# Optimization experiments

Measured on AMD Instinct MI355X. Metric: run time of the kernel, lower is better.

The kernel has to match this reference:

```python
import jax, jax.numpy as jnp
import numpy as np

N_NODES = 50000
N_EDGES = 800000
IN_CH, HID_CH, OUT_CH = 128, 128, 40


def setup_inputs() -> dict:
    key = jax.random.key(0)
    k1, k2, k3, k4 = jax.random.split(key, 4)
    x = jax.random.normal(k1, (N_NODES, IN_CH), dtype=jnp.float32)
    edge_index = jax.random.randint(k2, (2, N_EDGES), 0, N_NODES, dtype=jnp.int64)
    # Glorot-ish init for linear weights
    W1 = jax.random.normal(k3, (IN_CH, HID_CH), dtype=jnp.float32) / np.sqrt(IN_CH)
    b1 = jnp.zeros((HID_CH,), dtype=jnp.float32)
    W2 = jax.random.normal(k4, (HID_CH, OUT_CH), dtype=jnp.float32) / np.sqrt(HID_CH)
    b2 = jnp.zeros((OUT_CH,), dtype=jnp.float32)
    return {"x": x, "edge_index": edge_index, "W1": W1, "b1": b1, "W2": W2, "b2": b2}


def _gcn_conv(x, src, dst, W, b):
    # GCNConv(normalize=False): dense transform then sparse aggregation (scatter-add)
    h = x @ W                                   # [N, C_out]
    out = jax.ops.segment_sum(h[src], dst, num_segments=N_NODES)  # sum_{j->i} h[j]
    return out + b


def reference(x, edge_index, W1, b1, W2, b2):
    src, dst = edge_index[0], edge_index[1]
    h = _gcn_conv(x, src, dst, W1, b1)
    h = jax.nn.relu(h)
    # dropout is identity in eval mode
    h = _gcn_conv(h, src, dst, W2, b2)
    return jax.nn.log_softmax(h, axis=-1)
```

## Files before the change

kernel.cpp:

```cpp
#include <hip/hip_runtime.h>

#define NN 50000
#define NE 800000
#define NBKT 196
#define NBLK 256
#define EPB (NE / NBLK)
#define MATN (NBKT * NBLK)

using short8 = __attribute__((ext_vector_type(8))) short;
using f32x4  = __attribute__((ext_vector_type(4))) float;
union U4S8 { uint4 u; short8 v; };

__device__ __forceinline__ float lof(unsigned v) { return __uint_as_float(v << 16); }
__device__ __forceinline__ float hif(unsigned v) { return __uint_as_float(v & 0xffff0000u); }
__device__ __forceinline__ unsigned bf16rne(float f) {
    unsigned u = __float_as_uint(f);
    return (u + 0x7fffu + ((u >> 16) & 1u)) >> 16;
}
__device__ __forceinline__ unsigned pack2(float a, float b) {
    return bf16rne(a) | (bf16rne(b) << 16);
}
__device__ __forceinline__ unsigned fp8pack4(float a0, float a1, float a2, float a3) {
    int w = __builtin_amdgcn_cvt_pk_fp8_f32(a0, a1, 0, false);
    w = __builtin_amdgcn_cvt_pk_fp8_f32(a2, a3, w, true);
    return (unsigned)w;
}

__global__ __launch_bounds__(256) void binhist_k(const int* __restrict__ dst,
                                                 int* __restrict__ mat,
                                                 const float* __restrict__ W1,
                                                 const float* __restrict__ W2,
                                                 unsigned* __restrict__ W1T,
                                                 unsigned* __restrict__ W2T) {
    __shared__ int hist[NBKT];
    const int tid = threadIdx.x;
    for (int i = tid; i < NBKT; i += 256) hist[i] = 0;

    const int g = blockIdx.x * 256 + tid;
    if (g < 8192) {
        const int n = g >> 6, k2 = (g & 63) * 2;
        W1T[g] = pack2(W1[k2 * 128 + n], W1[(k2 + 1) * 128 + n]);
    } else if (g < 8192 + 3072) {
        const int u = g - 8192;
        const int n = u >> 6;
        const int q0 = (u & 63) * 2, q1 = q0 + 1;
        const int c0 = (q0 & 7) * 16 + (q0 >> 3);
        const int c1 = (q1 & 7) * 16 + (q1 >> 3);
        W2T[u] = (n < 40) ? pack2(W2[c0 * 40 + n], W2[c1 * 40 + n]) : 0u;
    }
    __syncthreads();

    const int base = blockIdx.x * EPB;
    for (int e = base + tid; e < base + EPB; e += 256)
        atomicAdd(&hist[dst[e] >> 8], 1);
    __syncthreads();
    for (int i = tid; i < NBKT; i += 256)
        mat[i * NBLK + blockIdx.x] = hist[i];
}

__global__ __launch_bounds__(256) void scanscatter_k(const int* __restrict__ src,
                                                     const int* __restrict__ dst,
                                                     const int* __restrict__ mat,
                                                     unsigned* __restrict__ binned,
                                                     int* __restrict__ bucketoff) {
    __shared__ int tot[NBKT];
    __shared__ int cur[NBKT];
    __shared__ int sc[256];
    const int tid = threadIdx.x;
    const int lane = tid & 63;
    const int w = tid >> 6;
    const int b = blockIdx.x;
    for (int i = w; i < NBKT; i += 4) {
        int t = 0, p = 0;
#pragma unroll
        for (int c = 0; c < 4; ++c) {
            const int col = c * 64 + lane;
            const int v = mat[i * NBLK + col];
            t += v;
            p += (col < b) ? v : 0;
        }
#pragma unroll
        for (int off = 32; off; off >>= 1) {
            t += __shfl_xor(t, off, 64);
            p += __shfl_xor(p, off, 64);
        }
        if (lane == 0) { tot[i] = t; cur[i] = p; }
    }
    __syncthreads();
    const int v = (tid < NBKT) ? tot[tid] : 0;
    sc[tid] = v;
    __syncthreads();
#pragma unroll
    for (int off = 1; off < 256; off <<= 1) {
        int u = (tid >= off) ? sc[tid - off] : 0;
        __syncthreads();
        sc[tid] += u;
        __syncthreads();
    }
    const int excl = sc[tid] - v;
    if (tid < NBKT) cur[tid] += excl;
    if (b == 0) {
        if (tid < NBKT) bucketoff[tid] = excl;
        if (tid == 0) bucketoff[NBKT] = NE;
    }
    __syncthreads();
    const int base = b * EPB;
    for (int e = base + tid; e < base + EPB; e += 256) {
        const int d = dst[e];
        const int p = atomicAdd(&cur[d >> 8], 1);
        binned[p] = ((unsigned)(d & 255) << 16) | (unsigned)src[e];
    }
}

__global__ __launch_bounds__(256) void csrgemm1_k(const unsigned* __restrict__ binned,
                                                  const int* __restrict__ bucketoff,
                                                  int* __restrict__ rowoff,
                                                  unsigned short* __restrict__ eid,
                                                  const float* __restrict__ x,
                                                  const unsigned* __restrict__ W1T,
                                                  uint2* __restrict__ H1) {
    __shared__ int cnt[256];
    __shared__ int off[256];
    const int tid = threadIdx.x;
    if (blockIdx.x < NBKT) {
        const int b = blockIdx.x;
        const int beg = bucketoff[b];
        const int end = bucketoff[b + 1];
        cnt[tid] = 0;
        __syncthreads();
        for (int i = beg + tid; i < end; i += 256)
            atomicAdd(&cnt[(binned[i] >> 16) & 255u], 1);
        __syncthreads();
        const int v = cnt[tid];
        off[tid] = v;
        __syncthreads();
#pragma unroll
        for (int o = 1; o < 256; o <<= 1) {
            int u = (tid >= o) ? off[tid - o] : 0;
            __syncthreads();
            off[tid] += u;
            __syncthreads();
        }
        const int excl = off[tid] - v;
        const int node = b * 256 + tid;
        if (node <= NN) rowoff[node] = beg + excl;
        cnt[tid] = excl;
        __syncthreads();
        for (int i = beg + tid; i < end; i += 256) {
            const unsigned e = binned[i];
            const int p = atomicAdd(&cnt[(e >> 16) & 255u], 1);
            eid[beg + p] = (unsigned short)(e & 0xffffu);
        }
        return;
    }
    const int lane = tid & 63;
    const int cl = lane & 15;
    const int kh = lane >> 4;
    const int gw = ((blockIdx.x - NBKT) * 256 + tid) >> 6;

    short8 Bf[8][4];
#pragma unroll
    for (int c = 0; c < 8; ++c)
#pragma unroll
        for (int kc = 0; kc < 4; ++kc) {
            U4S8 tb;
            tb.u = *(const uint4*)(W1T + ((c * 16 + cl) * 128 + kc * 32 + kh * 8) / 2);
            Bf[c][kc] = tb.v;
        }

    for (int mt = gw; mt < 3125; mt += 1024) {
        const int r0 = mt * 16;
        const float* ap = x + (long)(r0 + cl) * 128 + kh * 8;
        f32x4 acc[8];
#pragma unroll
        for (int c = 0; c < 8; ++c) acc[c] = (f32x4){0.f, 0.f, 0.f, 0.f};
#pragma unroll
        for (int kc = 0; kc < 4; ++kc) {
            const float4 p0 = *(const float4*)(ap + kc * 32);
            const float4 p1 = *(const float4*)(ap + kc * 32 + 4);
            U4S8 af;
            af.u.x = pack2(p0.x, p0.y);
            af.u.y = pack2(p0.z, p0.w);
            af.u.z = pack2(p1.x, p1.y);
            af.u.w = pack2(p1.z, p1.w);
#pragma unroll
            for (int c = 0; c < 8; ++c)
                acc[c] = __builtin_amdgcn_mfma_f32_16x16x32_bf16(af.v, Bf[c][kc], acc[c], 0, 0, 0);
        }
#pragma unroll
        for (int j = 0; j < 4; ++j) {
            uint2 o;
            o.x = fp8pack4(acc[0][j], acc[1][j], acc[2][j], acc[3][j]);
            o.y = fp8pack4(acc[4][j], acc[5][j], acc[6][j], acc[7][j]);
            H1[(long)(r0 + kh * 4 + j) * 16 + cl] = o;
        }
    }
}

__global__ __launch_bounds__(256) void gather1_k(const uint4* __restrict__ H1,
                                                 const int* __restrict__ rowoff,
                                                 const unsigned short* __restrict__ eid,
                                                 const float* __restrict__ b1,
                                                 uint4* __restrict__ h) {
    const int n = blockIdx.x * 4 + (threadIdx.x >> 6);
    const int lane = threadIdx.x & 63;
    const int g = lane >> 3;
    const int cl = lane & 7;
    const int beg = rowoff[n], end = rowoff[n + 1];
    float a[16];
#pragma unroll
    for (int i = 0; i < 16; ++i) a[i] = 0.f;

#define ACC16(v)                                                             \
    {                                                                        \
        auto t0 = __builtin_amdgcn_cvt_pk_f32_fp8((int)(v).x, false);        \
        auto t1 = __builtin_amdgcn_cvt_pk_f32_fp8((int)(v).x, true);         \
        auto t2 = __builtin_amdgcn_cvt_pk_f32_fp8((int)(v).y, false);        \
        auto t3 = __builtin_amdgcn_cvt_pk_f32_fp8((int)(v).y, true);         \
        auto t4 = __builtin_amdgcn_cvt_pk_f32_fp8((int)(v).z, false);        \
        auto t5 = __builtin_amdgcn_cvt_pk_f32_fp8((int)(v).z, true);         \
        auto t6 = __builtin_amdgcn_cvt_pk_f32_fp8((int)(v).w, false);        \
        auto t7 = __builtin_amdgcn_cvt_pk_f32_fp8((int)(v).w, true);         \
        a[0] += t0[0];  a[1] += t0[1];  a[2] += t1[0];  a[3] += t1[1];       \
        a[4] += t2[0];  a[5] += t2[1];  a[6] += t3[0];  a[7] += t3[1];       \
        a[8] += t4[0];  a[9] += t4[1];  a[10] += t5[0]; a[11] += t5[1];      \
        a[12] += t6[0]; a[13] += t6[1]; a[14] += t7[0]; a[15] += t7[1];      \
    }

    int k = beg;
    for (; k + 15 < end; k += 16) {
        const uint4 vA = H1[eid[k + g] * 8 + cl];
        const uint4 vB = H1[eid[k + 8 + g] * 8 + cl];
        ACC16(vA);
        ACC16(vB);
    }
    for (; k + 7 < end; k += 8) {
        const uint4 v = H1[eid[k + g] * 8 + cl];
        ACC16(v);
    }
    if (k + g < end) {
        const uint4 v = H1[eid[k + g] * 8 + cl];
        ACC16(v);
    }
#undef ACC16

#pragma unroll
    for (int i = 0; i < 16; ++i) {
        a[i] += __shfl_xor(a[i], 8, 64);
        a[i] += __shfl_xor(a[i], 16, 64);
        a[i] += __shfl_xor(a[i], 32, 64);
    }
    if (lane < 8) {
        float r[16];
#pragma unroll
        for (int i = 0; i < 16; ++i)
            r[i] = fmaxf(a[i] + b1[(i & 7) * 16 + cl * 2 + (i >> 3)], 0.f);
        uint4 o1, o2;
        o1.x = pack2(r[0], r[1]);  o1.y = pack2(r[2], r[3]);
        o1.z = pack2(r[4], r[5]);  o1.w = pack2(r[6], r[7]);
        o2.x = pack2(r[8], r[9]);  o2.y = pack2(r[10], r[11]);
        o2.z = pack2(r[12], r[13]); o2.w = pack2(r[14], r[15]);
        h[n * 16 + cl * 2] = o1;
        h[n * 16 + cl * 2 + 1] = o2;
    }
}

__global__ __launch_bounds__(256) void gemm2_k(const unsigned* __restrict__ h,
                                               const unsigned* __restrict__ W2T,
                                               unsigned short* __restrict__ H2) {
    const int lane = threadIdx.x & 63;
    const int cl = lane & 15;
    const int kh = lane >> 4;
    const int gw = (blockIdx.x * 256 + threadIdx.x) >> 6;

    short8 Bf[3][4];
#pragma unroll
    for (int c = 0; c < 3; ++c)
#pragma unroll
        for (int kc = 0; kc < 4; ++kc) {
            U4S8 tb;
            tb.u = *(const uint4*)(W2T + ((c * 16 + cl) * 128 + kc * 32 + kh * 8) / 2);
            Bf[c][kc] = tb.v;
        }

    for (int mt = gw; mt < 3125; mt += 1024) {
        const int r0 = mt * 16;
        const unsigned* ap = h + (long)(r0 + cl) * 64 + kh * 4;
        f32x4 acc[3];
#pragma unroll
        for (int c = 0; c < 3; ++c) acc[c] = (f32x4){0.f, 0.f, 0.f, 0.f};
#pragma unroll
        for (int kc = 0; kc < 4; ++kc) {
            U4S8 af;
            af.u = *(const uint4*)(ap + kc * 16);
#pragma unroll
            for (int c = 0; c < 3; ++c)
                acc[c] = __builtin_amdgcn_mfma_f32_16x16x32_bf16(af.v, Bf[c][kc], acc[c], 0, 0, 0);
        }
        unsigned short* hp = H2 + (long)(r0 + kh * 4) * 64;
#pragma unroll
        for (int c = 0; c < 3; ++c) {
            const int col = c * 16 + cl;
            if (col < 40) {
#pragma unroll
                for (int j = 0; j < 4; ++j)
                    hp[j * 64 + col] = (unsigned short)bf16rne(acc[c][j]);
            }
        }
    }
}

__global__ __launch_bounds__(256) void gather2_k(const uint4* __restrict__ H2,
                                                 const int* __restrict__ rowoff,
                                                 const unsigned short* __restrict__ eid,
                                                 const float* __restrict__ b2,
                                                 float* __restrict__ out) {
    const int n = blockIdx.x * 4 + (threadIdx.x >> 6);
    const int lane = threadIdx.x & 63;
    const int g = lane / 5;
    const int c4 = lane - g * 5;
    const int beg = rowoff[n], end = rowoff[n + 1];
    float a0 = 0.f, a1 = 0.f, a2 = 0.f, a3 = 0.f, a4 = 0.f, a5 = 0.f, a6 = 0.f, a7 = 0.f;
    if (g < 12) {
        int k = beg + g;
        for (; k + 12 < end; k += 24) {
            const uint4 v0 = H2[eid[k] * 8 + c4];
            const uint4 v1 = H2[eid[k + 12] * 8 + c4];
            a0 += lof(v0.x) + lof(v1.x); a1 += hif(v0.x) + hif(v1.x);
            a2 += lof(v0.y) + lof(v1.y); a3 += hif(v0.y) + hif(v1.y);
            a4 += lof(v0.z) + lof(v1.z); a5 += hif(v0.z) + hif(v1.z);
            a6 += lof(v0.w) + lof(v1.w); a7 += hif(v0.w) + hif(v1.w);
        }
        if (k < end) {
            const uint4 v = H2[eid[k] * 8 + c4];
            a0 += lof(v.x); a1 += hif(v.x);
            a2 += lof(v.y); a3 += hif(v.y);
            a4 += lof(v.z); a5 += hif(v.z);
            a6 += lof(v.w); a7 += hif(v.w);
        }
    }
#define FOLD1(A, D) A += __shfl(A, lane + (D), 64)
#define FOLD2(A) A += __shfl(A, lane + 5, 64) + __shfl(A, lane + 10, 64)
    FOLD1(a0, 30); FOLD1(a1, 30); FOLD1(a2, 30); FOLD1(a3, 30);
    FOLD1(a4, 30); FOLD1(a5, 30); FOLD1(a6, 30); FOLD1(a7, 30);
    FOLD1(a0, 15); FOLD1(a1, 15); FOLD1(a2, 15); FOLD1(a3, 15);
    FOLD1(a4, 15); FOLD1(a5, 15); FOLD1(a6, 15); FOLD1(a7, 15);
    FOLD2(a0); FOLD2(a1); FOLD2(a2); FOLD2(a3);
    FOLD2(a4); FOLD2(a5); FOLD2(a6); FOLD2(a7);
#undef FOLD1
#undef FOLD2

    const bool act = (lane < 5);
    float4 bA = {0.f, 0.f, 0.f, 0.f}, bB = {0.f, 0.f, 0.f, 0.f};
    if (act) {
        bA = ((const float4*)b2)[lane * 2];
        bB = ((const float4*)b2)[lane * 2 + 1];
    }
    const float v0 = a0 + bA.x, v1 = a1 + bA.y, v2 = a2 + bA.z, v3 = a3 + bA.w;
    const float v4 = a4 + bB.x, v5 = a5 + bB.y, v6 = a6 + bB.z, v7 = a7 + bB.w;
    float m = act ? fmaxf(fmaxf(fmaxf(v0, v1), fmaxf(v2, v3)),
                          fmaxf(fmaxf(v4, v5), fmaxf(v6, v7))) : -INFINITY;
#pragma unroll
    for (int off = 32; off; off >>= 1) m = fmaxf(m, __shfl_xor(m, off, 64));
    float e = act ? (expf(v0 - m) + expf(v1 - m) + expf(v2 - m) + expf(v3 - m) +
                     expf(v4 - m) + expf(v5 - m) + expf(v6 - m) + expf(v7 - m)) : 0.f;
#pragma unroll
    for (int off = 32; off; off >>= 1) e += __shfl_xor(e, off, 64);
    const float ls = logf(e);
    if (act) {
        float4 oA = {v0 - m - ls, v1 - m - ls, v2 - m - ls, v3 - m - ls};
        float4 oB = {v4 - m - ls, v5 - m - ls, v6 - m - ls, v7 - m - ls};
        float4* op = (float4*)(out + (long)n * 40 + lane * 8);
        op[0] = oA;
        op[1] = oB;
    }
}

extern "C" void kernel_launch(void* const* d_in, const int* in_sizes, int n_in,
                              void* d_out, int out_size, void* d_ws, size_t ws_size,
                              hipStream_t stream) {
    const float* x  = (const float*)d_in[0];
    const int*   ei = (const int*)d_in[1];
    const float* W1 = (const float*)d_in[2];
    const float* b1 = (const float*)d_in[3];
    const float* W2 = (const float*)d_in[4];
    const float* b2 = (const float*)d_in[5];
    const int* src = ei;
    const int* dst = ei + NE;

    unsigned* H1   = (unsigned*)d_ws;
    unsigned* h    = H1 + (size_t)NN * 32;
    unsigned* H2   = h + (size_t)NN * 64;
    unsigned* W1T  = H2 + (size_t)NN * 32;
    unsigned* W2T  = W1T + 8192;
    int* mat       = (int*)(W2T + 3072);
    int* bucketoff = mat + MATN;
    int* rowoff    = bucketoff + NBKT + 1;
    unsigned short* eid = (unsigned short*)(rowoff + NN + 1);
    unsigned* binned = h;
    float* out     = (float*)d_out;

    binhist_k<<<NBLK, 256, 0, stream>>>(dst, mat, W1, W2, W1T, W2T);
    scanscatter_k<<<NBLK, 256, 0, stream>>>(src, dst, mat, binned, bucketoff);
    csrgemm1_k<<<NBKT + 256, 256, 0, stream>>>(binned, bucketoff, rowoff, eid,
                                               x, W1T, (uint2*)H1);
    gather1_k<<<12500, 256, 0, stream>>>((const uint4*)H1, rowoff, eid, b1, (uint4*)h);
    gemm2_k<<<256, 256, 0, stream>>>(h, W2T, (unsigned short*)H2);
    gather2_k<<<12500, 256, 0, stream>>>((const uint4*)H2, rowoff, eid, b2, out);
}
```

Measured before the change: 129.4 us.

## Split fused scan-scatter into reduce, scan-finalize and scatter kernels

Replaces the single scan+scatter kernel, in which every block redundantly re-read the whole 196x256 histogram matrix and scanned it, with a three-kernel scheme. A per-bucket reduction computes totals, a second kernel scans them and writes exclusive per-block offsets back into the matrix, and the scatter kernel just loads its precomputed offsets. This removes the redundant matrix reads and the per-block scan from the scatter path, at the cost of two extra kernel launches and their serialization.

```diff
diff --git a/kernel.cpp b/kernel.cpp
--- a/kernel.cpp
+++ b/kernel.cpp
@@ -58,53 +58,62 @@
         mat[i * NBLK + blockIdx.x] = hist[i];
 }
 
-__global__ __launch_bounds__(256) void scanscatter_k(const int* __restrict__ src,
-                                                     const int* __restrict__ dst,
-                                                     const int* __restrict__ mat,
-                                                     unsigned* __restrict__ binned,
-                                                     int* __restrict__ bucketoff) {
-    __shared__ int tot[NBKT];
+__global__ __launch_bounds__(256) void reduce_k(const int* __restrict__ mat,
+                                                int* __restrict__ blocksum) {
+    int v = mat[blockIdx.x * NBLK + threadIdx.x];
+#pragma unroll
+    for (int off = 32; off; off >>= 1) v += __shfl_xor(v, off, 64);
+    __shared__ int ws[4];
+    if ((threadIdx.x & 63) == 0) ws[threadIdx.x >> 6] = v;
+    __syncthreads();
+    if (threadIdx.x == 0) blocksum[blockIdx.x] = ws[0] + ws[1] + ws[2] + ws[3];
+}
+
+__global__ __launch_bounds__(256) void scanfin_k(int* __restrict__ mat,
+                                                 const int* __restrict__ blocksum,
+                                                 int* __restrict__ bucketoff) {
+    __shared__ int bs[256];
+    __shared__ int sm[256];
+    const int t = threadIdx.x;
+    const int b = blockIdx.x;
+    const int mybs = (t < NBKT) ? blocksum[t] : 0;
+    bs[t] = mybs;
+    __syncthreads();
+#pragma unroll
+    for (int off = 1; off < 256; off <<= 1) {
+        int u = (t >= off) ? bs[t - off] : 0;
+        __syncthreads();
+        bs[t] += u;
+        __syncthreads();
+    }
+    if (b == 0) {
+        if (t < NBKT) bucketoff[t] = bs[t] - mybs;
+        if (t == 0) bucketoff[NBKT] = NE;
+    }
+    const int boff = bs[b] - blocksum[b];
+
+    const int v = mat[b * NBLK + t];
+    sm[t] = v;
+    __syncthreads();
+#pragma unroll
+    for (int off = 1; off < 256; off <<= 1) {
+        int u = (t >= off) ? sm[t - off] : 0;
+        __syncthreads();
+        sm[t] += u;
+        __syncthreads();
+    }
+    mat[b * NBLK + t] = boff + sm[t] - v;
+}
+
+__global__ __launch_bounds__(256) void scatter_k(const int* __restrict__ src,
+                                                 const int* __restrict__ dst,
+                                                 const int* __restrict__ mat,
+                                                 unsigned* __restrict__ binned) {
     __shared__ int cur[NBKT];
-    __shared__ int sc[256];
     const int tid = threadIdx.x;
-    const int lane = tid & 63;
-    const int w = tid >> 6;
-    const int b = blockIdx.x;
-    for (int i = w; i < NBKT; i += 4) {
-        int t = 0, p = 0;
-#pragma unroll
-        for (int c = 0; c < 4; ++c) {
-            const int col = c * 64 + lane;
-            const int v = mat[i * NBLK + col];
-            t += v;
-            p += (col < b) ? v : 0;
-        }
-#pragma unroll
-        for (int off = 32; off; off >>= 1) {
-            t += __shfl_xor(t, off, 64);
-            p += __shfl_xor(p, off, 64);
-        }
-        if (lane == 0) { tot[i] = t; cur[i] = p; }
-    }
-    __syncthreads();
-    const int v = (tid < NBKT) ? tot[tid] : 0;
-    sc[tid] = v;
-    __syncthreads();
-#pragma unroll
-    for (int off = 1; off < 256; off <<= 1) {
-        int u = (tid >= off) ? sc[tid - off] : 0;
-        __syncthreads();
-        sc[tid] += u;
-        __syncthreads();
-    }
-    const int excl = sc[tid] - v;
-    if (tid < NBKT) cur[tid] += excl;
-    if (b == 0) {
-        if (tid < NBKT) bucketoff[tid] = excl;
-        if (tid == 0) bucketoff[NBKT] = NE;
-    }
-    __syncthreads();
-    const int base = b * EPB;
+    for (int i = tid; i < NBKT; i += 256) cur[i] = mat[i * NBLK + blockIdx.x];
+    __syncthreads();
+    const int base = blockIdx.x * EPB;
     for (int e = base + tid; e < base + EPB; e += 256) {
         const int d = dst[e];
         const int p = atomicAdd(&cur[d >> 8], 1);
@@ -394,14 +403,17 @@
     unsigned* W1T  = H2 + (size_t)NN * 32;
     unsigned* W2T  = W1T + 8192;
     int* mat       = (int*)(W2T + 3072);
-    int* bucketoff = mat + MATN;
+    int* blocksum  = mat + MATN;
+    int* bucketoff = blocksum + 256;
     int* rowoff    = bucketoff + NBKT + 1;
     unsigned short* eid = (unsigned short*)(rowoff + NN + 1);
     unsigned* binned = h;
     float* out     = (float*)d_out;
 
     binhist_k<<<NBLK, 256, 0, stream>>>(dst, mat, W1, W2, W1T, W2T);
-    scanscatter_k<<<NBLK, 256, 0, stream>>>(src, dst, mat, binned, bucketoff);
+    reduce_k<<<NBKT, 256, 0, stream>>>(mat, blocksum);
+    scanfin_k<<<NBKT, 256, 0, stream>>>(mat, blocksum, bucketoff);
+    scatter_k<<<NBLK, 256, 0, stream>>>(src, dst, mat, binned);
     csrgemm1_k<<<NBKT + 256, 256, 0, stream>>>(binned, bucketoff, rowoff, eid,
                                                x, W1T, (uint2*)H1);
     gather1_k<<<12500, 256, 0, stream>>>((const uint4*)H1, rowoff, eid, b1, (uint4*)h);
```

After: 110.5 us. 1.17x faster.
